# Optimization experiments

Measured on AMD Instinct MI355X. Metric: run time of the kernel, lower is better.

Reference implementation:

```python
import jax, jax.numpy as jnp
import numpy as np

LATENT = 64
HID = 64
IN_DIM = HID + 1  # 65
SLOPE = 0.2
EPS = 1e-8


def setup_inputs() -> dict:
    key = jax.random.key(0)
    ks = jax.random.split(key, 9)
    x = jax.random.normal(ks[0], (8192, LATENT, IN_DIM), dtype=jnp.float32)
    def init_w(k, shape, fan_in):
        return jax.random.uniform(k, shape, jnp.float32, -1.0, 1.0) / np.sqrt(fan_in)
    # Per-latent stacked MLP params: 3 LeakyReLU layers + final linear to scalar
    W0 = init_w(ks[1], (LATENT, HID, IN_DIM), IN_DIM)
    b0 = init_w(ks[2], (LATENT, HID), IN_DIM)
    W1 = init_w(ks[3], (LATENT, HID, HID), HID)
    b1 = init_w(ks[4], (LATENT, HID), HID)
    W2 = init_w(ks[5], (LATENT, HID, HID), HID)
    b2 = init_w(ks[6], (LATENT, HID), HID)
    W3 = init_w(ks[7], (LATENT, 1, HID), HID)
    b3 = init_w(ks[8], (LATENT, 1), HID)
    return {"x": x, "W0": W0, "b0": b0, "W1": W1, "b1": b1,
            "W2": W2, "b2": b2, "W3": W3, "b3": b3}


def _flow_single(w0, b0, w1, b1, w2, b2, w3, b3, xi):
    # xi: [B, IN_DIM] -> residual [B], d(out)/d(xi[:, -1]) [B]
    def f(z):
        h = jax.nn.leaky_relu(z @ w0.T + b0, SLOPE)
        h = jax.nn.leaky_relu(h @ w1.T + b1, SLOPE)
        h = jax.nn.leaky_relu(h @ w2.T + b2, SLOPE)
        return h @ w3.T + b3  # [B, 1]
    # only the last column of the Jacobian is used -> single batched JVP
    tan = jnp.zeros_like(xi).at[:, -1].set(1.0)
    out, dout = jax.jvp(f, (xi,), (tan,))
    return out[:, 0], dout[:, 0]


def reference(x, W0, b0, W1, b1, W2, b2, W3, b3):
    B = x.shape[0]
    # vmap over the latent axis (independent MLP per latent)
    residuals, dJ = jax.vmap(_flow_single,
                             in_axes=(0, 0, 0, 0, 0, 0, 0, 0, 1),
                             out_axes=(1, 1))(W0, b0, W1, b1, W2, b2, W3, b3, x)
    # residuals: [B, LATENT]; dJ: [B, LATENT]
    logabsdet = jnp.sum(jnp.log(jnp.abs(dJ) + EPS), axis=1)  # [B]
    return residuals.reshape(B, -1), logabsdet.reshape(B, -1)
```

## Files before the change

kernel.cpp:

```cpp
#include <hip/hip_runtime.h>
#include <hip/hip_bf16.h>
#include <cmath>

#define LATENTS 64
#define HID 64
#define IN_DIM 65
#define SLOPE 0.2f
#define FEPS 1e-8f
#define RPB 128
#define WBYTES 53248
#define W65_BYTE (64 * WBYTES)

#define A_OF_SLOT(s) ((((((s) >> 2) & 1) * 2 + ((s) >> 5)) * 16) + ((((s) >> 3) & 3) * 4) + ((s) & 3))

typedef __attribute__((ext_vector_type(8))) short short8;
typedef __attribute__((ext_vector_type(4))) float f32x4;
typedef __attribute__((address_space(1))) const unsigned GASU;
typedef __attribute__((address_space(3))) unsigned LASU;

__device__ __forceinline__ unsigned asu(float f){ return __builtin_bit_cast(unsigned, f); }
__device__ __forceinline__ float    asf(unsigned u){ return __builtin_bit_cast(float, u); }
__device__ __forceinline__ unsigned bfu(float f){
    return (unsigned)__builtin_bit_cast(unsigned short, __float2bfloat16(f));
}

__device__ __forceinline__ void split8v(const float* f, short8& hi, short8& lo){
    unsigned hw[4], lw[4];
#pragma unroll
    for (int w = 0; w < 4; ++w){
        float a = f[2 * w], b = f[2 * w + 1];
        unsigned ha = asu(a) & 0xFFFF0000u, hb = asu(b) & 0xFFFF0000u;
        float la = a - asf(ha), lb = b - asf(hb);
        hw[w] = (ha >> 16) | hb;
        lw[w] = bfu(la) | (bfu(lb) << 16);
    }
    uint4 h4{hw[0], hw[1], hw[2], hw[3]}, l4{lw[0], lw[1], lw[2], lw[3]};
    hi = __builtin_bit_cast(short8, h4);
    lo = __builtin_bit_cast(short8, l4);
}

__device__ __forceinline__ f32x4 mfma_(short8 a, short8 b, f32x4 c){
    return __builtin_amdgcn_mfma_f32_16x16x32_bf16(a, b, c, 0, 0, 0);
}

__global__ void lad_init_kernel(float* __restrict__ lad, int n){
    int i = blockIdx.x * blockDim.x + threadIdx.x;
    if (i < n) lad[i] = 0.0f;
}

__global__ __launch_bounds__(64)
void w_prep_kernel(const float* __restrict__ W0, const float* __restrict__ W1,
                   const float* __restrict__ W2, const float* __restrict__ W3,
                   char* __restrict__ ws)
{
    const int b = blockIdx.x;
    const int L = threadIdx.x;
    const int c  = L & 15;
    const int kb = (L >> 4) * 8;
    if (b < 192){
        const int l = b / 3, d = b - 3 * l;
        const float* Wd = (d == 0) ? W0 + (size_t)l * 64 * IN_DIM
                        : (d == 1) ? W1 + (size_t)l * 4096
                                   : W2 + (size_t)l * 4096;
        const int K = (d == 0) ? IN_DIM : 64;
#pragma unroll
        for (int ks = 0; ks < 2; ++ks)
#pragma unroll
            for (int ct = 0; ct < 4; ++ct){
                float wf[8];
#pragma unroll
                for (int j = 0; j < 8; ++j){
                    const int s = ks * 32 + kb + j;
                    const int a = (d == 0) ? s : A_OF_SLOT(s);
                    wf[j] = Wd[(size_t)(ct * 16 + c) * K + a];
                }
                short8 wh, wl;
                split8v(wf, wh, wl);
                char* base = ws + (size_t)l * WBYTES + d * 16384 + (ks * 4 + ct) * 1024 + L * 16;
                *(short8*)base            = wh;
                *(short8*)(base + 8192)   = wl;
            }
    } else {
        const int l = b - 192;
#pragma unroll
        for (int ks = 0; ks < 2; ++ks){
            float wf[8];
#pragma unroll
            for (int j = 0; j < 8; ++j)
                wf[j] = (c == 0) ? W3[l * 64 + A_OF_SLOT(ks * 32 + kb + j)] : 0.0f;
            short8 wh, wl;
            split8v(wf, wh, wl);
            char* base = ws + (size_t)l * WBYTES + 49152 + ks * 1024 + L * 16;
            *(short8*)base          = wh;
            *(short8*)(base + 2048) = wl;
        }
        ((float*)(ws + W65_BYTE))[l * 64 + L] =
            W0[(size_t)l * 64 * IN_DIM + L * IN_DIM + 64];
    }
}

__global__ __launch_bounds__(256, 2)
void flow_mfma_kernel(const float* __restrict__ x,
                      const float* __restrict__ b0, const float* __restrict__ b1,
                      const float* __restrict__ b2, const float* __restrict__ b3,
                      const char* __restrict__ ws,
                      float* __restrict__ out_res, float* __restrict__ out_lad)
{
    __shared__ __attribute__((aligned(16))) char wlds[WBYTES];

    const int l   = blockIdx.y;
    const int tid = threadIdx.x;
    const int L   = tid & 63;
    const int wv  = tid >> 6;
    const int u   = L >> 4;
    const int g0  = blockIdx.x * RPB + wv * 32 + (L & 15);
    const int g1  = g0 + 16;

    const char* gsrc = ws + (size_t)l * WBYTES;
#pragma unroll
    for (int i = 0; i < 13; ++i){
        const int off = (i * 256 + wv * 64) * 16;
        __builtin_amdgcn_global_load_lds((GASU*)(gsrc + off + L * 16),
                                         (LASU*)(wlds + off), 16, 0, 0);
    }

    const float* xg0 = x + ((size_t)g0 * LATENTS + l) * IN_DIM;
    const float* xg1 = x + ((size_t)g1 * LATENTS + l) * IN_DIM;
    float xv[2][16];
    float x65r[2];
#pragma unroll
    for (int j = 0; j < 8; ++j){
        xv[0][j]     = xg0[8 * u + j];
        xv[0][8 + j] = xg0[32 + 8 * u + j];
        xv[1][j]     = xg1[8 * u + j];
        xv[1][8 + j] = xg1[32 + 8 * u + j];
    }
    x65r[0] = xg0[64];
    x65r[1] = xg1[64];

    const float* w65p = (const float*)(ws + W65_BYTE) + l * 64;
    float4 w65v[4], bv0[4], bv1[4], bv2[4];
#pragma unroll
    for (int ct = 0; ct < 4; ++ct){
        w65v[ct] = *(const float4*)(w65p + ct * 16 + u * 4);
        bv0[ct]  = *(const float4*)(b0 + l * 64 + ct * 16 + u * 4);
        bv1[ct]  = *(const float4*)(b1 + l * 64 + ct * 16 + u * 4);
        bv2[ct]  = *(const float4*)(b2 + l * 64 + ct * 16 + u * 4);
    }

    short8 bh[2][2], bl2[2][2], th2[2][2], tl2[2][2];
#pragma unroll
    for (int t = 0; t < 2; ++t){
        split8v(&xv[t][0], bh[t][0], bl2[t][0]);
        split8v(&xv[t][8], bh[t][1], bl2[t][1]);
    }

    __syncthreads();

    f32x4 ha[2][4], ta[2][4];

    auto ldw = [&](int d, int ks, int ct, short8& wh, short8& wl){
        const char* p = wlds + d * 16384 + (ks * 4 + ct) * 1024 + (L << 4);
        wh = *(const short8*)p;
        wl = *(const short8*)(p + 8192);
    };
    auto repack = [&](int t, const float v[4][4], short8 (&hi)[2][2], short8 (&lo)[2][2]){
#pragma unroll
        for (int ks = 0; ks < 2; ++ks){
            float f8[8] = {v[ks][0], v[ks][1], v[ks][2], v[ks][3],
                           v[2 + ks][0], v[2 + ks][1], v[2 + ks][2], v[2 + ks][3]};
            split8v(f8, hi[t][ks], lo[t][ks]);
        }
    };

    {
#pragma unroll
        for (int t = 0; t < 2; ++t)
#pragma unroll
            for (int ct = 0; ct < 4; ++ct)
                ha[t][ct] = (f32x4){bv0[ct].x, bv0[ct].y, bv0[ct].z, bv0[ct].w};
#pragma unroll
        for (int ks = 0; ks < 2; ++ks){
#pragma unroll
            for (int ct = 0; ct < 4; ++ct){
                short8 wh, wl;
                ldw(0, ks, ct, wh, wl);
                __builtin_amdgcn_s_setprio(1);
#pragma unroll
                for (int t = 0; t < 2; ++t){
                    ha[t][ct] = mfma_(wh, bh[t][ks],  ha[t][ct]);
                    ha[t][ct] = mfma_(wh, bl2[t][ks], ha[t][ct]);
                    ha[t][ct] = mfma_(wl, bh[t][ks],  ha[t][ct]);
                }
                __builtin_amdgcn_s_setprio(0);
            }
        }
#pragma unroll
        for (int t = 0; t < 2; ++t){
            float hv[4][4], tv[4][4];
#pragma unroll
            for (int ct = 0; ct < 4; ++ct){
                const float wa[4] = {w65v[ct].x, w65v[ct].y, w65v[ct].z, w65v[ct].w};
#pragma unroll
                for (int i = 0; i < 4; ++i){
                    float z = fmaf(x65r[t], wa[i], ha[t][ct][i]);
                    hv[ct][i] = fmaxf(z, SLOPE * z);
                    tv[ct][i] = (z >= 0.0f) ? wa[i] : SLOPE * wa[i];
                }
            }
            repack(t, hv, bh, bl2);
            repack(t, tv, th2, tl2);
        }
    }

    auto dense2 = [&](int d, const float4 (&bv)[4]){
#pragma unroll
        for (int t = 0; t < 2; ++t)
#pragma unroll
            for (int ct = 0; ct < 4; ++ct){
                ha[t][ct] = (f32x4){bv[ct].x, bv[ct].y, bv[ct].z, bv[ct].w};
                ta[t][ct] = (f32x4){0.f, 0.f, 0.f, 0.f};
            }
#pragma unroll
        for (int ks = 0; ks < 2; ++ks){
#pragma unroll
            for (int ct = 0; ct < 4; ++ct){
                short8 wh, wl;
                ldw(d, ks, ct, wh, wl);
                __builtin_amdgcn_s_setprio(1);
#pragma unroll
                for (int t = 0; t < 2; ++t){
                    ha[t][ct] = mfma_(wh, bh[t][ks],  ha[t][ct]);
                    ha[t][ct] = mfma_(wh, bl2[t][ks], ha[t][ct]);
                    ha[t][ct] = mfma_(wl, bh[t][ks],  ha[t][ct]);
                    ta[t][ct] = mfma_(wh, th2[t][ks], ta[t][ct]);
                    ta[t][ct] = mfma_(wh, tl2[t][ks], ta[t][ct]);
                    ta[t][ct] = mfma_(wl, th2[t][ks], ta[t][ct]);
                }
                __builtin_amdgcn_s_setprio(0);
            }
        }
#pragma unroll
        for (int t = 0; t < 2; ++t){
            float hv[4][4], tv[4][4];
#pragma unroll
            for (int ct = 0; ct < 4; ++ct)
#pragma unroll
                for (int i = 0; i < 4; ++i){
                    float z  = ha[t][ct][i];
                    float zt = ta[t][ct][i];
                    hv[ct][i] = fmaxf(z, SLOPE * z);
                    tv[ct][i] = (z >= 0.0f) ? zt : SLOPE * zt;
                }
            repack(t, hv, bh, bl2);
            repack(t, tv, th2, tl2);
        }
    };
    dense2(1, bv1);
    dense2(2, bv2);

    {
        f32x4 so[2], sd[2];
#pragma unroll
        for (int t = 0; t < 2; ++t){
            so[t] = (f32x4){0.f, 0.f, 0.f, 0.f};
            sd[t] = (f32x4){0.f, 0.f, 0.f, 0.f};
        }
#pragma unroll
        for (int ks = 0; ks < 2; ++ks){
            const char* p = wlds + 49152 + ks * 1024 + (L << 4);
            short8 wh = *(const short8*)p;
            short8 wl = *(const short8*)(p + 2048);
            __builtin_amdgcn_s_setprio(1);
#pragma unroll
            for (int t = 0; t < 2; ++t){
                so[t] = mfma_(wh, bh[t][ks],  so[t]);
                so[t] = mfma_(wh, bl2[t][ks], so[t]);
                so[t] = mfma_(wl, bh[t][ks],  so[t]);
                sd[t] = mfma_(wh, th2[t][ks], sd[t]);
                sd[t] = mfma_(wh, tl2[t][ks], sd[t]);
                sd[t] = mfma_(wl, th2[t][ks], sd[t]);
            }
            __builtin_amdgcn_s_setprio(0);
        }
        if (u == 0){
            const float b3v = b3[l];
            out_res[(size_t)g0 * LATENTS + l] = so[0][0] + b3v;
            out_res[(size_t)g1 * LATENTS + l] = so[1][0] + b3v;
            atomicAdd(&out_lad[g0], __logf(fabsf(sd[0][0]) + FEPS));
            atomicAdd(&out_lad[g1], __logf(fabsf(sd[1][0]) + FEPS));
        }
    }
}

extern "C" void kernel_launch(void* const* d_in, const int* in_sizes, int n_in,
                              void* d_out, int out_size, void* d_ws, size_t ws_size,
                              hipStream_t stream)
{
    const float* x  = (const float*)d_in[0];
    const float* W0 = (const float*)d_in[1];
    const float* b0 = (const float*)d_in[2];
    const float* W1 = (const float*)d_in[3];
    const float* b1 = (const float*)d_in[4];
    const float* W2 = (const float*)d_in[5];
    const float* b2 = (const float*)d_in[6];
    const float* W3 = (const float*)d_in[7];
    const float* b3 = (const float*)d_in[8];

    const int B = in_sizes[0] / (LATENTS * IN_DIM);
    float* out_res = (float*)d_out;
    float* out_lad = out_res + (size_t)B * LATENTS;
    char*  wsp     = (char*)d_ws;

    lad_init_kernel<<<dim3((B + 255) / 256), dim3(256), 0, stream>>>(out_lad, B);
    w_prep_kernel<<<dim3(256), dim3(64), 0, stream>>>(W0, W1, W2, W3, wsp);
    flow_mfma_kernel<<<dim3(B / RPB, LATENTS), dim3(256), 0, stream>>>(
        x, b0, b1, b2, b3, wsp, out_res, out_lad);
}
```

Measured before the change: 87.51 us.

## Drop low-bf16 tangent term and double block size to 512 threads

The tangent activations are now packed as a single bf16 value instead of a hi/lo split. This removes one MFMA per tangent product and the lo-part packing, which lowers tangent precision. Blocks also grow from 256 to 512 threads (256 rows each), so every block's LDS weight copy is amortised over twice as many rows. The launch bounds request 4 blocks per CU, which may limit registers, and the weight-to-LDS copy loop is adjusted to match.

```diff
diff --git a/kernel.cpp b/kernel.cpp
--- a/kernel.cpp
+++ b/kernel.cpp
@@ -7,7 +7,7 @@
 #define IN_DIM 65
 #define SLOPE 0.2f
 #define FEPS 1e-8f
-#define RPB 128
+#define RPB 256
 #define WBYTES 53248
 #define W65_BYTE (64 * WBYTES)
 
@@ -37,6 +37,15 @@
     uint4 h4{hw[0], hw[1], hw[2], hw[3]}, l4{lw[0], lw[1], lw[2], lw[3]};
     hi = __builtin_bit_cast(short8, h4);
     lo = __builtin_bit_cast(short8, l4);
+}
+
+__device__ __forceinline__ short8 pack8v(const float* f){
+    unsigned w[4];
+#pragma unroll
+    for (int i = 0; i < 4; ++i)
+        w[i] = bfu(f[2 * i]) | (bfu(f[2 * i + 1]) << 16);
+    uint4 p{w[0], w[1], w[2], w[3]};
+    return __builtin_bit_cast(short8, p);
 }
 
 __device__ __forceinline__ f32x4 mfma_(short8 a, short8 b, f32x4 c){
@@ -99,7 +108,7 @@
     }
 }
 
-__global__ __launch_bounds__(256, 2)
+__global__ __launch_bounds__(512, 4)
 void flow_mfma_kernel(const float* __restrict__ x,
                       const float* __restrict__ b0, const float* __restrict__ b1,
                       const float* __restrict__ b2, const float* __restrict__ b3,
@@ -118,10 +127,11 @@
 
     const char* gsrc = ws + (size_t)l * WBYTES;
 #pragma unroll
-    for (int i = 0; i < 13; ++i){
-        const int off = (i * 256 + wv * 64) * 16;
-        __builtin_amdgcn_global_load_lds((GASU*)(gsrc + off + L * 16),
-                                         (LASU*)(wlds + off), 16, 0, 0);
+    for (int i = 0; i < 7; ++i){
+        const int base = i * 512 + wv * 64;
+        if (base * 16 < WBYTES)
+            __builtin_amdgcn_global_load_lds((GASU*)(gsrc + (base + L) * 16),
+                                             (LASU*)(wlds + base * 16), 16, 0, 0);
     }
 
     const float* xg0 = x + ((size_t)g0 * LATENTS + l) * IN_DIM;
@@ -148,7 +158,7 @@
         bv2[ct]  = *(const float4*)(b2 + l * 64 + ct * 16 + u * 4);
     }
 
-    short8 bh[2][2], bl2[2][2], th2[2][2], tl2[2][2];
+    short8 bh[2][2], bl2[2][2], th2[2][2];
 #pragma unroll
     for (int t = 0; t < 2; ++t){
         split8v(&xv[t][0], bh[t][0], bl2[t][0]);
@@ -172,6 +182,14 @@
             split8v(f8, hi[t][ks], lo[t][ks]);
         }
     };
+    auto repackt = [&](int t, const float v[4][4], short8 (&hi)[2][2]){
+#pragma unroll
+        for (int ks = 0; ks < 2; ++ks){
+            float f8[8] = {v[ks][0], v[ks][1], v[ks][2], v[ks][3],
+                           v[2 + ks][0], v[2 + ks][1], v[2 + ks][2], v[2 + ks][3]};
+            hi[t][ks] = pack8v(f8);
+        }
+    };
 
     {
 #pragma unroll
@@ -209,7 +227,7 @@
                 }
             }
             repack(t, hv, bh, bl2);
-            repack(t, tv, th2, tl2);
+            repackt(t, tv, th2);
         }
     }
 
@@ -234,7 +252,6 @@
                     ha[t][ct] = mfma_(wh, bl2[t][ks], ha[t][ct]);
                     ha[t][ct] = mfma_(wl, bh[t][ks],  ha[t][ct]);
                     ta[t][ct] = mfma_(wh, th2[t][ks], ta[t][ct]);
-                    ta[t][ct] = mfma_(wh, tl2[t][ks], ta[t][ct]);
                     ta[t][ct] = mfma_(wl, th2[t][ks], ta[t][ct]);
                 }
                 __builtin_amdgcn_s_setprio(0);
@@ -253,7 +270,7 @@
                     tv[ct][i] = (z >= 0.0f) ? zt : SLOPE * zt;
                 }
             repack(t, hv, bh, bl2);
-            repack(t, tv, th2, tl2);
+            repackt(t, tv, th2);
         }
     };
     dense2(1, bv1);
@@ -278,7 +295,6 @@
                 so[t] = mfma_(wh, bl2[t][ks], so[t]);
                 so[t] = mfma_(wl, bh[t][ks],  so[t]);
                 sd[t] = mfma_(wh, th2[t][ks], sd[t]);
-                sd[t] = mfma_(wh, tl2[t][ks], sd[t]);
                 sd[t] = mfma_(wl, th2[t][ks], sd[t]);
             }
             __builtin_amdgcn_s_setprio(0);
@@ -314,6 +330,6 @@
 
     lad_init_kernel<<<dim3((B + 255) / 256), dim3(256), 0, stream>>>(out_lad, B);
     w_prep_kernel<<<dim3(256), dim3(64), 0, stream>>>(W0, W1, W2, W3, wsp);
-    flow_mfma_kernel<<<dim3(B / RPB, LATENTS), dim3(256), 0, stream>>>(
+    flow_mfma_kernel<<<dim3(B / RPB, LATENTS), dim3(512), 0, stream>>>(
         x, b0, b1, b2, b3, wsp, out_res, out_lad);
 }
```

Result: slower. 113.2 us (+29.4%).
